# Kernel tuning notes

Hardware: AMD Instinct MI355X
Metric: run time of the kernel (lower is better)

The kernel has to match this reference:

```python
import jax, jax.numpy as jnp
import numpy as np

DIM = 1024
HEADS = 16
DIM_HEAD = 64
INNER = HEADS * DIM_HEAD  # 1024
RANK = 16
ALPHA = 8.0
LORA_SCALE = ALPHA / RANK  # 0.5
NUM_PATCHES = 256
NUM_FRAMES = 8
T = NUM_PATCHES * NUM_FRAMES  # 2048
B = 2
MEM = 16
EPS = 1e-5


def _block_causal_mask(num_patches, num_frames):
    # generate_mask_matrix: causal across frames, full within a frame
    tril = np.tril(np.ones((num_frames, num_frames), dtype=np.int32))
    m = np.kron(tril, np.ones((num_patches, num_patches), dtype=np.int32))
    return jnp.asarray(m[None, None])  # [1,1,T,T]


def setup_inputs() -> dict:
    key = jax.random.key(0)
    ks = jax.random.split(key, 16)
    s_in = 1.0 / np.sqrt(DIM)
    s_r = 1.0 / np.sqrt(RANK)
    return {
        "x": jax.random.normal(ks[0], (B, T, DIM), jnp.float32),
        "memory_tokens": jax.random.normal(ks[1], (B, MEM, DIM), jnp.float32),
        "ln_g": jnp.ones((DIM,), jnp.float32),
        "ln_b": jnp.zeros((DIM,), jnp.float32),
        "w_qkv": jax.random.normal(ks[2], (DIM, 3 * INNER), jnp.float32) * s_in,
        "qA": jax.random.normal(ks[3], (DIM, RANK), jnp.float32) * s_in,
        "qB": jax.random.normal(ks[4], (RANK, INNER), jnp.float32) * s_r * 0.02,
        "kA": jax.random.normal(ks[5], (DIM, RANK), jnp.float32) * s_in,
        "kB": jax.random.normal(ks[6], (RANK, INNER), jnp.float32) * s_r * 0.02,
        "vA": jax.random.normal(ks[7], (DIM, RANK), jnp.float32) * s_in,
        "vB": jax.random.normal(ks[8], (RANK, INNER), jnp.float32) * s_r * 0.02,
        "w_out": jax.random.normal(ks[9], (INNER, DIM), jnp.float32) / np.sqrt(INNER),
        "b_out": jnp.zeros((DIM,), jnp.float32),
        "outA": jax.random.normal(ks[10], (INNER, RANK), jnp.float32) / np.sqrt(INNER),
        "outB": jax.random.normal(ks[11], (RANK, DIM), jnp.float32) * s_r * 0.02,
        "bias_mask": _block_causal_mask(NUM_PATCHES, NUM_FRAMES),
    }


def _lora(x, A, Bm):
    return LORA_SCALE * ((x @ A) @ Bm)


def reference(x, memory_tokens, ln_g, ln_b, w_qkv, qA, qB, kA, kB, vA, vB,
              w_out, b_out, outA, outB, bias_mask):
    # LayerNorm
    mu = jnp.mean(x, axis=-1, keepdims=True)
    var = jnp.var(x, axis=-1, keepdims=True)
    xn = (x - mu) * jax.lax.rsqrt(var + EPS) * ln_g + ln_b

    qkv = xn @ w_qkv  # [B,T,3*INNER]
    q, k, v = jnp.split(qkv, 3, axis=-1)
    # LoRA deltas (memory_tokens enables the LoRA path)
    q = q + _lora(xn, qA, qB)
    k = k + _lora(xn, kA, kB)
    v = v + _lora(xn, vA, vB)

    def to_heads(t):
        b, n, _ = t.shape
        return t.reshape(b, n, HEADS, DIM_HEAD).transpose(0, 2, 1, 3)  # b h n d

    q, k, v = to_heads(q), to_heads(k), to_heads(v)
    scale = DIM_HEAD ** -0.5
    dots = jnp.einsum('bhid,bhjd->bhij', q, k) * scale  # [B,H,T,T]
    dots = jnp.where(bias_mask[:, :, :q.shape[2], :q.shape[2]] == 0, -jnp.inf, dots)
    attn = jax.nn.softmax(dots, axis=-1)  # dropout p=0.0
    out = jnp.einsum('bhij,bhjd->bhid', attn, v)
    out = out.transpose(0, 2, 1, 3).reshape(x.shape[0], x.shape[1], INNER)
    out = out @ w_out + b_out
    out = out + _lora(out, outA, outB)  # lora_on_out
    return out
```

## Files before the change

### kernel.cpp

```cpp
#include <hip/hip_runtime.h>


#define DIMSZ 1024
#define TSEQ  2048
#define MTOK  4096

typedef __attribute__((ext_vector_type(8))) short bf16x8;
typedef __attribute__((ext_vector_type(4))) short bf16x4;
typedef __attribute__((ext_vector_type(4))) float f32x4;

__device__ __forceinline__ unsigned short f2bf(float f) {
  unsigned int u = __float_as_uint(f);
  u += 0x7fffu + ((u >> 16) & 1u);
  return (unsigned short)(u >> 16);
}
__device__ __forceinline__ float bf2f(unsigned short s) {
  return __uint_as_float(((unsigned int)s) << 16);
}
__device__ __forceinline__ unsigned int cvtpk_bf16(float a, float b) {
  unsigned int d;
  asm("v_cvt_pk_bf16_f32 %0, %1, %2" : "=v"(d) : "v"(a), "v"(b));
  return d;
}
__device__ __forceinline__ void gload16(const void* g, void* l) {
  __builtin_amdgcn_global_load_lds((const __attribute__((address_space(1))) void*)g,
                                   (__attribute__((address_space(3))) void*)l, 16, 0, 0);
}

__global__ __launch_bounds__(256) void ln_kernel(const float* __restrict__ x,
    const float* __restrict__ g, const float* __restrict__ b,
    unsigned short* __restrict__ xn) {
  int row = blockIdx.x;
  int tid = threadIdx.x;
  const float4* xr = (const float4*)(x + (size_t)row * DIMSZ);
  float4 v = xr[tid];
  float s  = v.x + v.y + v.z + v.w;
  float s2 = v.x*v.x + v.y*v.y + v.z*v.z + v.w*v.w;
  #pragma unroll
  for (int off = 32; off > 0; off >>= 1) {
    s  += __shfl_xor(s, off, 64);
    s2 += __shfl_xor(s2, off, 64);
  }
  __shared__ float red[8];
  int wid = tid >> 6, lane = tid & 63;
  if (lane == 0) { red[wid] = s; red[wid + 4] = s2; }
  __syncthreads();
  s  = red[0] + red[1] + red[2] + red[3];
  s2 = red[4] + red[5] + red[6] + red[7];
  float mu  = s * (1.0f / DIMSZ);
  float var = s2 * (1.0f / DIMSZ) - mu * mu;
  float rstd = rsqrtf(var + 1e-5f);
  float4 gg = ((const float4*)g)[tid];
  float4 bb = ((const float4*)b)[tid];
  ushort4 o;
  o.x = f2bf((v.x - mu) * rstd * gg.x + bb.x);
  o.y = f2bf((v.y - mu) * rstd * gg.y + bb.y);
  o.z = f2bf((v.z - mu) * rstd * gg.z + bb.z);
  o.w = f2bf((v.w - mu) * rstd * gg.w + bb.w);
  ((ushort4*)(xn + (size_t)row * DIMSZ))[tid] = o;
}

__global__ __launch_bounds__(64) void woutA_kernel(const float* __restrict__ w_out,
    const float* __restrict__ outA, float* __restrict__ WA) {
  int k = blockIdx.x;
  int l = threadIdx.x;
  float a[16];
  #pragma unroll
  for (int r = 0; r < 16; ++r) a[r] = 0.f;
  for (int c = l; c < DIMSZ; c += 64) {
    float w = w_out[(size_t)k * DIMSZ + c];
    const float* ap = outA + (size_t)c * 16;
    #pragma unroll
    for (int r = 0; r < 16; ++r) a[r] += w * ap[r];
  }
  #pragma unroll
  for (int r = 0; r < 16; ++r) {
    #pragma unroll
    for (int off = 32; off > 0; off >>= 1) a[r] += __shfl_xor(a[r], off, 64);
  }
  if (l < 16) WA[k * 16 + l] = a[l];
}

__global__ __launch_bounds__(256) void beff_kernel(const float* __restrict__ b_out,
    const float* __restrict__ outA, const float* __restrict__ outB,
    float* __restrict__ beff) {
  int tid = threadIdx.x, wid = tid >> 6, lane = tid & 63;
  float a[16];
  #pragma unroll
  for (int r = 0; r < 16; ++r) a[r] = 0.f;
  for (int c = tid; c < DIMSZ; c += 256) {
    float bo = b_out[c];
    const float* ap = outA + (size_t)c * 16;
    #pragma unroll
    for (int r = 0; r < 16; ++r) a[r] += bo * ap[r];
  }
  #pragma unroll
  for (int r = 0; r < 16; ++r) {
    #pragma unroll
    for (int off = 32; off > 0; off >>= 1) a[r] += __shfl_xor(a[r], off, 64);
  }
  __shared__ float sh[4][16];
  if (lane == 0) {
    #pragma unroll
    for (int r = 0; r < 16; ++r) sh[wid][r] = a[r];
  }
  __syncthreads();
  __shared__ float tt[16];
  if (tid < 16) tt[tid] = sh[0][tid] + sh[1][tid] + sh[2][tid] + sh[3][tid];
  __syncthreads();
  for (int n = tid; n < DIMSZ; n += 256) {
    float l = 0.f;
    #pragma unroll
    for (int r = 0; r < 16; ++r) l += tt[r] * outB[(size_t)r * DIMSZ + n];
    beff[n] = b_out[n] + 0.5f * l;
  }
}

__global__ __launch_bounds__(256) void foldT4_kernel(
    const float* __restrict__ w_qkv, const float* __restrict__ w_out,
    const float* __restrict__ qA, const float* __restrict__ qB,
    const float* __restrict__ kA, const float* __restrict__ kB,
    const float* __restrict__ vA, const float* __restrict__ vB,
    const float* __restrict__ WA, const float* __restrict__ outB,
    unsigned short* __restrict__ WqkvT, unsigned short* __restrict__ WoutT) {
  __shared__ float Bs[16][64];
  __shared__ unsigned short Ts[64][72];
  int z = blockIdx.z;
  const float *W, *A, *Bf;
  unsigned short* Wt;
  int ldw, col_off;
  if (z == 0)      { W = w_qkv; ldw = 3072; col_off = 0;    A = qA; Bf = qB;   Wt = WqkvT; }
  else if (z == 1) { W = w_qkv; ldw = 3072; col_off = 1024; A = kA; Bf = kB;   Wt = WqkvT + 1048576; }
  else if (z == 2) { W = w_qkv; ldw = 3072; col_off = 2048; A = vA; Bf = vB;   Wt = WqkvT + 2097152; }
  else             { W = w_out; ldw = 1024; col_off = 0;    A = WA; Bf = outB; Wt = WoutT; }
  int n0 = blockIdx.x * 64, k0 = blockIdx.y * 64;
  int tx = threadIdx.x, ty = threadIdx.y;
  for (int r = ty; r < 16; r += 4) Bs[r][tx] = Bf[(size_t)r * DIMSZ + n0 + tx];
  __syncthreads();
  for (int k = ty; k < 64; k += 4) {
    int kk = k0 + k;
    float w = W[(size_t)kk * ldw + col_off + n0 + tx];
    const float* Ar = A + (size_t)kk * 16;
    float lora = 0.f;
    #pragma unroll
    for (int r = 0; r < 16; ++r) lora += Ar[r] * Bs[r][tx];
    Ts[tx][k] = f2bf(w + 0.5f * lora);
  }
  __syncthreads();
  for (int n = ty; n < 64; n += 4)
    Wt[(size_t)(n0 + n) * DIMSZ + k0 + tx] = Ts[n][tx];
}

template<int MODE>
__global__ __launch_bounds__(256) void gemm_kernel(
    const unsigned short* __restrict__ Abf, const unsigned short* __restrict__ Bt,
    int K,
    unsigned short* __restrict__ Qo, unsigned short* __restrict__ Ko,
    unsigned short* __restrict__ Vto,
    const float* __restrict__ bias, float* __restrict__ Cout) {
  __shared__ __align__(16) char As[128 * 64 * 2];
  __shared__ __align__(16) char Bs[128 * 64 * 2];
  int n0 = blockIdx.x * 128;
  int m0 = blockIdx.y * 128;
  int tid = threadIdx.x;
  int wid = tid >> 6, lane = tid & 63;
  int wr = wid >> 1, wc = wid & 1;
  int hi = lane >> 4;
  f32x4 acc[4][4];
  #pragma unroll
  for (int i = 0; i < 4; ++i)
    #pragma unroll
    for (int j = 0; j < 4; ++j) acc[i][j] = (f32x4){0.f, 0.f, 0.f, 0.f};

  const char* gA = (const char*)Abf;
  const char* gB = (const char*)Bt;
  int Kb2 = K * 2;
  int nkt = K >> 6;
  for (int kt = 0; kt < nkt; ++kt) {
    #pragma unroll
    for (int j = 0; j < 4; ++j) {
      int it = wid * 4 + j;
      int p = it * 1024 + lane * 16;
      int row = p >> 7, colb = p & 127;
      int L = colb ^ ((row & 7) << 4);
      gload16(gA + (size_t)(m0 + row) * Kb2 + kt * 128 + L, As + it * 1024);
      gload16(gB + (size_t)(n0 + row) * Kb2 + kt * 128 + L, Bs + it * 1024);
    }
    __syncthreads();
    #pragma unroll
    for (int ks = 0; ks < 2; ++ks) {
      int kb = ks * 64 + hi * 16;
      bf16x8 af[4], bfr[4];
      #pragma unroll
      for (int m = 0; m < 4; ++m) {
        int row = wr * 64 + m * 16 + (lane & 15);
        af[m] = *(const bf16x8*)(As + row * 128 + (kb ^ ((row & 7) << 4)));
      }
      #pragma unroll
      for (int n = 0; n < 4; ++n) {
        int row = wc * 64 + n * 16 + (lane & 15);
        bfr[n] = *(const bf16x8*)(Bs + row * 128 + (kb ^ ((row & 7) << 4)));
      }
      __builtin_amdgcn_s_setprio(1);
      #pragma unroll
      for (int n = 0; n < 4; ++n)
        #pragma unroll
        for (int m = 0; m < 4; ++m)
          acc[n][m] = __builtin_amdgcn_mfma_f32_16x16x32_bf16(bfr[n], af[m], acc[n][m], 0, 0, 0);
      __builtin_amdgcn_s_setprio(0);
    }
    __syncthreads();
  }

  if (MODE == 0) {
    int sec  = n0 >> 10;
    int nloc = (n0 & 1023) + wc * 64;
    int h = nloc >> 6;
    int mbase = m0 + wr * 64;
    #pragma unroll
    for (int m = 0; m < 4; ++m) {
      int gm = mbase + m * 16 + (lane & 15);
      int bb = gm >> 11, t = gm & 2047;
      #pragma unroll
      for (int n = 0; n < 4; ++n) {
        int dloc = n * 16 + hi * 4;
        if (sec == 2) {
          #pragma unroll
          for (int r = 0; r < 4; ++r)
            Vto[((size_t)((bb * 16 + h) * 64 + dloc + r)) * TSEQ + t] = f2bf(acc[n][m][r]);
        } else {
          bf16x4 o;
          #pragma unroll
          for (int r = 0; r < 4; ++r) o[r] = (short)f2bf(acc[n][m][r]);
          size_t idx = ((size_t)(bb * 16 + h) * TSEQ + t) * 64 + dloc;
          *(bf16x4*)((sec == 0 ? Qo : Ko) + idx) = o;
        }
      }
    }
  } else {
    int mbase = m0 + wr * 64;
    int nbase = n0 + wc * 64;
    #pragma unroll
    for (int m = 0; m < 4; ++m) {
      int t = mbase + m * 16 + (lane & 15);
      #pragma unroll
      for (int n = 0; n < 4; ++n) {
        int c = nbase + n * 16 + hi * 4;
        float4 bs = *(const float4*)(bias + c);
        float4 o;
        o.x = acc[n][m][0] + bs.x;
        o.y = acc[n][m][1] + bs.y;
        o.z = acc[n][m][2] + bs.z;
        o.w = acc[n][m][3] + bs.w;
        *(float4*)(Cout + (size_t)t * DIMSZ + c) = o;
      }
    }
  }
}

__global__ __launch_bounds__(256, 4) void attn_kernel(
    const unsigned short* __restrict__ Qg, const unsigned short* __restrict__ Kg,
    const unsigned short* __restrict__ Vt, unsigned short* __restrict__ Orow) {
  __shared__ __align__(16) char KsB[2][64 * 128];
  __shared__ __align__(16) char VsB[2][64 * 128];
  __shared__ __align__(16) char Ps[4][16 * 128];
  int bh = blockIdx.x;
  int y  = blockIdx.y;
  int qt = (y < 16) ? (31 - y) : (y - 16);
  int b = bh >> 4, h = bh & 15;
  int tid = threadIdx.x, wid = tid >> 6, lane = tid & 63;
  int hi = lane >> 4, lo = lane & 15;
  const char* Qb = (const char*)(Qg + (size_t)bh * TSEQ * 64);
  const char* Kb = (const char*)(Kg + (size_t)bh * TSEQ * 64);
  const char* Vb = (const char*)(Vt + (size_t)bh * 64 * TSEQ);
  int q0 = qt * 64;

  int srow = tid >> 3;
  int scol = ((tid & 7) << 4) ^ ((srow & 7) << 4);

  const float qscale = 0.18033688f;
  bf16x8 qf[2];
  {
    int row = q0 + wid * 16 + lo;
    #pragma unroll
    for (int ks = 0; ks < 2; ++ks) {
      bf16x8 raw = *(const bf16x8*)(Qb + (size_t)row * 128 + ks * 64 + hi * 16);
      bf16x8 sc;
      #pragma unroll
      for (int i = 0; i < 8; ++i)
        sc[i] = (short)f2bf(bf2f((unsigned short)raw[i]) * qscale);
      qf[ks] = sc;
    }
  }

  f32x4 Oacc[4];
  #pragma unroll
  for (int df = 0; df < 4; ++df) Oacc[df] = (f32x4){0.f, 0.f, 0.f, 0.f};
  float mrun = -INFINITY, lrun = 0.f;

  char* Pw = Ps[wid];
  char* pbase = Pw + lo * 128;
  int pswz = (lo & 7) << 4;

  int nkt = ((qt >> 2) + 1) << 2;

  {
    const char* ksrc = Kb + (size_t)srow * 128 + scol;
    gload16(ksrc,               KsB[0] + tid * 16);
    gload16(ksrc + 32 * 128,    KsB[0] + tid * 16 + 4096);
    const char* vsrc = Vb + (size_t)srow * (TSEQ * 2) + scol;
    gload16(vsrc,               VsB[0] + tid * 16);
    gload16(vsrc + 32 * (TSEQ * 2), VsB[0] + tid * 16 + 4096);
  }

  for (int kt = 0; kt < nkt; ++kt) {
    __syncthreads();
    if (kt + 1 < nkt) {
      int k0n = (kt + 1) << 6;
      char* kd = KsB[(kt + 1) & 1];
      const char* ksrc = Kb + (size_t)(k0n + srow) * 128 + scol;
      gload16(ksrc,            kd + tid * 16);
      gload16(ksrc + 32 * 128, kd + tid * 16 + 4096);
    }
    if (kt) {
      char* vd = VsB[kt & 1];
      const char* vsrc = Vb + (size_t)srow * (TSEQ * 2) + (kt << 7) + scol;
      gload16(vsrc,                   vd + tid * 16);
      gload16(vsrc + 32 * (TSEQ * 2), vd + tid * 16 + 4096);
    }
    const char* Kbuf = KsB[kt & 1];

    f32x4 s[4];
    #pragma unroll
    for (int nf = 0; nf < 4; ++nf) s[nf] = (f32x4){0.f, 0.f, 0.f, 0.f};
    #pragma unroll
    for (int ks = 0; ks < 2; ++ks) {
      int kb = ks * 64 + hi * 16;
      bf16x8 kf[4];
      #pragma unroll
      for (int nf = 0; nf < 4; ++nf) {
        int row = nf * 16 + lo;
        kf[nf] = *(const bf16x8*)(Kbuf + row * 128 + (kb ^ ((row & 7) << 4)));
      }
      __builtin_amdgcn_s_setprio(1);
      #pragma unroll
      for (int nf = 0; nf < 4; ++nf)
        s[nf] = __builtin_amdgcn_mfma_f32_16x16x32_bf16(kf[nf], qf[ks], s[nf], 0, 0, 0);
      __builtin_amdgcn_s_setprio(0);
    }

    if (kt) {
      const char* Vbuf = VsB[(kt - 1) & 1];
      #pragma unroll
      for (int ks2 = 0; ks2 < 2; ++ks2) {
        int kb = ks2 * 64 + hi * 16;
        bf16x8 pf = *(const bf16x8*)(Pw + lo * 128 + (kb ^ pswz));
        bf16x8 vf[4];
        #pragma unroll
        for (int df = 0; df < 4; ++df) {
          int row = df * 16 + lo;
          vf[df] = *(const bf16x8*)(Vbuf + row * 128 + (kb ^ ((row & 7) << 4)));
        }
        __builtin_amdgcn_s_setprio(1);
        #pragma unroll
        for (int df = 0; df < 4; ++df)
          Oacc[df] = __builtin_amdgcn_mfma_f32_16x16x32_bf16(vf[df], pf, Oacc[df], 0, 0, 0);
        __builtin_amdgcn_s_setprio(0);
      }
    }

    float a0 = fmaxf(fmaxf(s[0][0], s[0][1]), fmaxf(s[0][2], s[0][3]));
    float a1 = fmaxf(fmaxf(s[1][0], s[1][1]), fmaxf(s[1][2], s[1][3]));
    float a2 = fmaxf(fmaxf(s[2][0], s[2][1]), fmaxf(s[2][2], s[2][3]));
    float a3 = fmaxf(fmaxf(s[3][0], s[3][1]), fmaxf(s[3][2], s[3][3]));
    float mx = fmaxf(fmaxf(a0, a1), fmaxf(a2, a3));
    mx = fmaxf(mx, __shfl_xor(mx, 16, 64));
    mx = fmaxf(mx, __shfl_xor(mx, 32, 64));

    if (!__all(mx <= mrun + 8.0f)) {
      float mn = fmaxf(mrun, mx);
      float al = exp2f(mrun - mn);
      mrun = mn;
      lrun *= al;
      #pragma unroll
      for (int df = 0; df < 4; ++df)
        #pragma unroll
        for (int r = 0; r < 4; ++r) Oacc[df][r] *= al;
    }

    float rs0 = 0.f, rs1 = 0.f, rs2 = 0.f, rs3 = 0.f;
    #pragma unroll
    for (int nf = 0; nf < 4; ++nf) {
      float p0 = exp2f(s[nf][0] - mrun);
      float p1 = exp2f(s[nf][1] - mrun);
      float p2 = exp2f(s[nf][2] - mrun);
      float p3 = exp2f(s[nf][3] - mrun);
      s[nf][0] = p0; s[nf][1] = p1; s[nf][2] = p2; s[nf][3] = p3;
      rs0 += p0; rs1 += p1; rs2 += p2; rs3 += p3;
    }
    lrun += (rs0 + rs1) + (rs2 + rs3);

    #pragma unroll
    for (int nf = 0; nf < 4; ++nf) {
      unsigned int w0 = cvtpk_bf16(s[nf][0], s[nf][1]);
      unsigned int w1 = cvtpk_bf16(s[nf][2], s[nf][3]);
      uint2 pr; pr.x = w0; pr.y = w1;
      *(uint2*)(pbase + ((nf * 32 + hi * 8) ^ pswz)) = pr;
    }
  }

  __syncthreads();
  {
    const char* Vbuf = VsB[(nkt - 1) & 1];
    #pragma unroll
    for (int ks2 = 0; ks2 < 2; ++ks2) {
      int kb = ks2 * 64 + hi * 16;
      bf16x8 pf = *(const bf16x8*)(Pw + lo * 128 + (kb ^ pswz));
      bf16x8 vf[4];
      #pragma unroll
      for (int df = 0; df < 4; ++df) {
        int row = df * 16 + lo;
        vf[df] = *(const bf16x8*)(Vbuf + row * 128 + (kb ^ ((row & 7) << 4)));
      }
      __builtin_amdgcn_s_setprio(1);
      #pragma unroll
      for (int df = 0; df < 4; ++df)
        Oacc[df] = __builtin_amdgcn_mfma_f32_16x16x32_bf16(vf[df], pf, Oacc[df], 0, 0, 0);
      __builtin_amdgcn_s_setprio(0);
    }
  }

  lrun += __shfl_xor(lrun, 16, 64);
  lrun += __shfl_xor(lrun, 32, 64);
  float inv = 1.0f / lrun;
  int t = q0 + wid * 16 + lo;
  size_t rowbase = ((size_t)(b * TSEQ + t)) * DIMSZ + h * 64;
  #pragma unroll
  for (int df = 0; df < 4; ++df) {
    bf16x4 o;
    #pragma unroll
    for (int r = 0; r < 4; ++r) o[r] = (short)f2bf(Oacc[df][r] * inv);
    *(bf16x4*)(Orow + rowbase + df * 16 + hi * 4) = o;
  }
}

extern "C" void kernel_launch(void* const* d_in, const int* in_sizes, int n_in,
                              void* d_out, int out_size, void* d_ws, size_t ws_size,
                              hipStream_t stream) {
  (void)in_sizes; (void)n_in; (void)out_size; (void)ws_size;
  const float* x     = (const float*)d_in[0];
  const float* ln_g  = (const float*)d_in[2];
  const float* ln_b  = (const float*)d_in[3];
  const float* w_qkv = (const float*)d_in[4];
  const float* qA    = (const float*)d_in[5];
  const float* qB    = (const float*)d_in[6];
  const float* kA    = (const float*)d_in[7];
  const float* kB    = (const float*)d_in[8];
  const float* vA    = (const float*)d_in[9];
  const float* vB    = (const float*)d_in[10];
  const float* w_out = (const float*)d_in[11];
  const float* b_out = (const float*)d_in[12];
  const float* outA  = (const float*)d_in[13];
  const float* outB  = (const float*)d_in[14];

  char* ws = (char*)d_ws;
  unsigned short* xn    = (unsigned short*)(ws);
  unsigned short* WqkvT = (unsigned short*)(ws + 8388608);
  unsigned short* WoutT = (unsigned short*)(ws + 14680064);
  float*          WA    = (float*)(ws + 16777216);
  float*          beff  = (float*)(ws + 16842752);
  unsigned short* Qb    = (unsigned short*)(ws + 16846848);
  unsigned short* Kb    = (unsigned short*)(ws + 25235456);
  unsigned short* Vtb   = (unsigned short*)(ws + 33624064);
  unsigned short* Orow  = xn;
  float* outp = (float*)d_out;

  ln_kernel<<<MTOK, 256, 0, stream>>>(x, ln_g, ln_b, xn);
  woutA_kernel<<<DIMSZ, 64, 0, stream>>>(w_out, outA, WA);
  beff_kernel<<<1, 256, 0, stream>>>(b_out, outA, outB, beff);
  dim3 fb(64, 4);
  foldT4_kernel<<<dim3(16, 16, 4), fb, 0, stream>>>(w_qkv, w_out, qA, qB, kA, kB,
                                                    vA, vB, WA, outB, WqkvT, WoutT);

  gemm_kernel<0><<<dim3(24, 32), 256, 0, stream>>>(xn, WqkvT, DIMSZ, Qb, Kb, Vtb, nullptr, nullptr);
  attn_kernel<<<dim3(32, 32), 256, 0, stream>>>(Qb, Kb, Vtb, Orow);
  gemm_kernel<1><<<dim3(8, 32), 256, 0, stream>>>(Orow, WoutT, DIMSZ, nullptr, nullptr, nullptr, beff, outp);
}
```

Measured before the change: 142.9 us.

## Use 32x32 MFMA in attention with two waves per block, fuse prep kernels

The attention kernel is restructured so each of two waves handles 32 query rows using 32x32x16 bf16 MFMAs instead of four waves using 16x16x32. This cuts the number of MFMA issues and cross-lane reductions, but raises per-wave register pressure and halves threads per block, which changes occupancy. Separately, the LayerNorm, W_out·outA and effective-bias kernels are merged into one launch to save launch overhead.

```diff
diff --git a/kernel.cpp b/kernel.cpp
--- a/kernel.cpp
+++ b/kernel.cpp
@@ -8,6 +8,7 @@
 typedef __attribute__((ext_vector_type(8))) short bf16x8;
 typedef __attribute__((ext_vector_type(4))) short bf16x4;
 typedef __attribute__((ext_vector_type(4))) float f32x4;
+typedef __attribute__((ext_vector_type(16))) float f32x16;
 
 __device__ __forceinline__ unsigned short f2bf(float f) {
   unsigned int u = __float_as_uint(f);
@@ -27,92 +28,88 @@
                                    (__attribute__((address_space(3))) void*)l, 16, 0, 0);
 }
 
-__global__ __launch_bounds__(256) void ln_kernel(const float* __restrict__ x,
-    const float* __restrict__ g, const float* __restrict__ b,
-    unsigned short* __restrict__ xn) {
-  int row = blockIdx.x;
-  int tid = threadIdx.x;
-  const float4* xr = (const float4*)(x + (size_t)row * DIMSZ);
-  float4 v = xr[tid];
-  float s  = v.x + v.y + v.z + v.w;
-  float s2 = v.x*v.x + v.y*v.y + v.z*v.z + v.w*v.w;
-  #pragma unroll
-  for (int off = 32; off > 0; off >>= 1) {
-    s  += __shfl_xor(s, off, 64);
-    s2 += __shfl_xor(s2, off, 64);
-  }
+__global__ __launch_bounds__(256) void prep_kernel(const float* __restrict__ x,
+    const float* __restrict__ g, const float* __restrict__ bln,
+    const float* __restrict__ w_out, const float* __restrict__ outA,
+    const float* __restrict__ b_out, const float* __restrict__ outB,
+    unsigned short* __restrict__ xn, float* __restrict__ WA,
+    float* __restrict__ beff) {
   __shared__ float red[8];
-  int wid = tid >> 6, lane = tid & 63;
-  if (lane == 0) { red[wid] = s; red[wid + 4] = s2; }
-  __syncthreads();
-  s  = red[0] + red[1] + red[2] + red[3];
-  s2 = red[4] + red[5] + red[6] + red[7];
-  float mu  = s * (1.0f / DIMSZ);
-  float var = s2 * (1.0f / DIMSZ) - mu * mu;
-  float rstd = rsqrtf(var + 1e-5f);
-  float4 gg = ((const float4*)g)[tid];
-  float4 bb = ((const float4*)b)[tid];
-  ushort4 o;
-  o.x = f2bf((v.x - mu) * rstd * gg.x + bb.x);
-  o.y = f2bf((v.y - mu) * rstd * gg.y + bb.y);
-  o.z = f2bf((v.z - mu) * rstd * gg.z + bb.z);
-  o.w = f2bf((v.w - mu) * rstd * gg.w + bb.w);
-  ((ushort4*)(xn + (size_t)row * DIMSZ))[tid] = o;
-}
-
-__global__ __launch_bounds__(64) void woutA_kernel(const float* __restrict__ w_out,
-    const float* __restrict__ outA, float* __restrict__ WA) {
-  int k = blockIdx.x;
-  int l = threadIdx.x;
-  float a[16];
-  #pragma unroll
-  for (int r = 0; r < 16; ++r) a[r] = 0.f;
-  for (int c = l; c < DIMSZ; c += 64) {
-    float w = w_out[(size_t)k * DIMSZ + c];
-    const float* ap = outA + (size_t)c * 16;
-    #pragma unroll
-    for (int r = 0; r < 16; ++r) a[r] += w * ap[r];
-  }
-  #pragma unroll
-  for (int r = 0; r < 16; ++r) {
-    #pragma unroll
-    for (int off = 32; off > 0; off >>= 1) a[r] += __shfl_xor(a[r], off, 64);
-  }
-  if (l < 16) WA[k * 16 + l] = a[l];
-}
-
-__global__ __launch_bounds__(256) void beff_kernel(const float* __restrict__ b_out,
-    const float* __restrict__ outA, const float* __restrict__ outB,
-    float* __restrict__ beff) {
+  __shared__ float sh[4][16];
+  __shared__ float tt[16];
+  int bid = blockIdx.x;
   int tid = threadIdx.x, wid = tid >> 6, lane = tid & 63;
-  float a[16];
-  #pragma unroll
-  for (int r = 0; r < 16; ++r) a[r] = 0.f;
-  for (int c = tid; c < DIMSZ; c += 256) {
-    float bo = b_out[c];
-    const float* ap = outA + (size_t)c * 16;
-    #pragma unroll
-    for (int r = 0; r < 16; ++r) a[r] += bo * ap[r];
-  }
-  #pragma unroll
-  for (int r = 0; r < 16; ++r) {
-    #pragma unroll
-    for (int off = 32; off > 0; off >>= 1) a[r] += __shfl_xor(a[r], off, 64);
-  }
-  __shared__ float sh[4][16];
-  if (lane == 0) {
-    #pragma unroll
-    for (int r = 0; r < 16; ++r) sh[wid][r] = a[r];
-  }
-  __syncthreads();
-  __shared__ float tt[16];
-  if (tid < 16) tt[tid] = sh[0][tid] + sh[1][tid] + sh[2][tid] + sh[3][tid];
-  __syncthreads();
-  for (int n = tid; n < DIMSZ; n += 256) {
-    float l = 0.f;
-    #pragma unroll
-    for (int r = 0; r < 16; ++r) l += tt[r] * outB[(size_t)r * DIMSZ + n];
-    beff[n] = b_out[n] + 0.5f * l;
+  if (bid < MTOK) {
+    int row = bid;
+    const float4* xr = (const float4*)(x + (size_t)row * DIMSZ);
+    float4 v = xr[tid];
+    float s  = v.x + v.y + v.z + v.w;
+    float s2 = v.x*v.x + v.y*v.y + v.z*v.z + v.w*v.w;
+    #pragma unroll
+    for (int off = 32; off > 0; off >>= 1) {
+      s  += __shfl_xor(s, off, 64);
+      s2 += __shfl_xor(s2, off, 64);
+    }
+    if (lane == 0) { red[wid] = s; red[wid + 4] = s2; }
+    __syncthreads();
+    s  = red[0] + red[1] + red[2] + red[3];
+    s2 = red[4] + red[5] + red[6] + red[7];
+    float mu  = s * (1.0f / DIMSZ);
+    float var = s2 * (1.0f / DIMSZ) - mu * mu;
+    float rstd = rsqrtf(var + 1e-5f);
+    float4 gg = ((const float4*)g)[tid];
+    float4 bb = ((const float4*)bln)[tid];
+    ushort4 o;
+    o.x = f2bf((v.x - mu) * rstd * gg.x + bb.x);
+    o.y = f2bf((v.y - mu) * rstd * gg.y + bb.y);
+    o.z = f2bf((v.z - mu) * rstd * gg.z + bb.z);
+    o.w = f2bf((v.w - mu) * rstd * gg.w + bb.w);
+    ((ushort4*)(xn + (size_t)row * DIMSZ))[tid] = o;
+  } else if (bid < MTOK + 256) {
+    int k = (bid - MTOK) * 4 + wid;
+    float a[16];
+    #pragma unroll
+    for (int r = 0; r < 16; ++r) a[r] = 0.f;
+    for (int c = lane; c < DIMSZ; c += 64) {
+      float w = w_out[(size_t)k * DIMSZ + c];
+      const float* ap = outA + (size_t)c * 16;
+      #pragma unroll
+      for (int r = 0; r < 16; ++r) a[r] += w * ap[r];
+    }
+    #pragma unroll
+    for (int r = 0; r < 16; ++r) {
+      #pragma unroll
+      for (int off = 32; off > 0; off >>= 1) a[r] += __shfl_xor(a[r], off, 64);
+    }
+    if (lane < 16) WA[k * 16 + lane] = a[lane];
+  } else {
+    float a[16];
+    #pragma unroll
+    for (int r = 0; r < 16; ++r) a[r] = 0.f;
+    for (int c = tid; c < DIMSZ; c += 256) {
+      float bo = b_out[c];
+      const float* ap = outA + (size_t)c * 16;
+      #pragma unroll
+      for (int r = 0; r < 16; ++r) a[r] += bo * ap[r];
+    }
+    #pragma unroll
+    for (int r = 0; r < 16; ++r) {
+      #pragma unroll
+      for (int off = 32; off > 0; off >>= 1) a[r] += __shfl_xor(a[r], off, 64);
+    }
+    if (lane == 0) {
+      #pragma unroll
+      for (int r = 0; r < 16; ++r) sh[wid][r] = a[r];
+    }
+    __syncthreads();
+    if (tid < 16) tt[tid] = sh[0][tid] + sh[1][tid] + sh[2][tid] + sh[3][tid];
+    __syncthreads();
+    for (int n = tid; n < DIMSZ; n += 256) {
+      float l = 0.f;
+      #pragma unroll
+      for (int r = 0; r < 16; ++r) l += tt[r] * outB[(size_t)r * DIMSZ + n];
+      beff[n] = b_out[n] + 0.5f * l;
+    }
   }
 }
 
@@ -258,123 +255,126 @@
   }
 }
 
-__global__ __launch_bounds__(256, 4) void attn_kernel(
+__global__ __launch_bounds__(128, 2) void attn_kernel(
     const unsigned short* __restrict__ Qg, const unsigned short* __restrict__ Kg,
     const unsigned short* __restrict__ Vt, unsigned short* __restrict__ Orow) {
   __shared__ __align__(16) char KsB[2][64 * 128];
   __shared__ __align__(16) char VsB[2][64 * 128];
-  __shared__ __align__(16) char Ps[4][16 * 128];
+  __shared__ __align__(16) char Pws[2][32 * 128];
   int bh = blockIdx.x;
   int y  = blockIdx.y;
   int qt = (y < 16) ? (31 - y) : (y - 16);
   int b = bh >> 4, h = bh & 15;
   int tid = threadIdx.x, wid = tid >> 6, lane = tid & 63;
-  int hi = lane >> 4, lo = lane & 15;
+  int l31 = lane & 31, hi1 = lane >> 5;
   const char* Qb = (const char*)(Qg + (size_t)bh * TSEQ * 64);
   const char* Kb = (const char*)(Kg + (size_t)bh * TSEQ * 64);
   const char* Vb = (const char*)(Vt + (size_t)bh * 64 * TSEQ);
   int q0 = qt * 64;
 
   int srow = tid >> 3;
-  int scol = ((tid & 7) << 4) ^ ((srow & 7) << 4);
+  int scs  = ((tid & 7) << 4) ^ ((srow & 7) << 4);
 
   const float qscale = 0.18033688f;
-  bf16x8 qf[2];
+  bf16x8 qf[4];
   {
-    int row = q0 + wid * 16 + lo;
-    #pragma unroll
-    for (int ks = 0; ks < 2; ++ks) {
-      bf16x8 raw = *(const bf16x8*)(Qb + (size_t)row * 128 + ks * 64 + hi * 16);
-      bf16x8 sc;
+    int qrow = q0 + wid * 32 + l31;
+    #pragma unroll
+    for (int kb = 0; kb < 4; ++kb) {
+      bf16x8 raw = *(const bf16x8*)(Qb + (size_t)qrow * 128 + kb * 32 + hi1 * 16);
+      bf16x8 scv;
       #pragma unroll
       for (int i = 0; i < 8; ++i)
-        sc[i] = (short)f2bf(bf2f((unsigned short)raw[i]) * qscale);
-      qf[ks] = sc;
-    }
-  }
-
-  f32x4 Oacc[4];
-  #pragma unroll
-  for (int df = 0; df < 4; ++df) Oacc[df] = (f32x4){0.f, 0.f, 0.f, 0.f};
+        scv[i] = (short)f2bf(bf2f((unsigned short)raw[i]) * qscale);
+      qf[kb] = scv;
+    }
+  }
+
+  f32x16 Oa[2];
+  Oa[0] = (f32x16)(0.f); Oa[1] = (f32x16)(0.f);
   float mrun = -INFINITY, lrun = 0.f;
 
-  char* Pw = Ps[wid];
-  char* pbase = Pw + lo * 128;
-  int pswz = (lo & 7) << 4;
+  char* Pw   = Pws[wid];
+  char* prow = Pw + l31 * 128;
+  int   pswz = (l31 & 7) << 4;
 
   int nkt = ((qt >> 2) + 1) << 2;
 
   {
-    const char* ksrc = Kb + (size_t)srow * 128 + scol;
-    gload16(ksrc,               KsB[0] + tid * 16);
-    gload16(ksrc + 32 * 128,    KsB[0] + tid * 16 + 4096);
-    const char* vsrc = Vb + (size_t)srow * (TSEQ * 2) + scol;
-    gload16(vsrc,               VsB[0] + tid * 16);
-    gload16(vsrc + 32 * (TSEQ * 2), VsB[0] + tid * 16 + 4096);
+    const char* ks = Kb + (size_t)srow * 128 + scs;
+    char* kd = KsB[0] + tid * 16;
+    gload16(ks, kd); gload16(ks + 2048, kd + 2048);
+    gload16(ks + 4096, kd + 4096); gload16(ks + 6144, kd + 6144);
+    const char* vs = Vb + (size_t)srow * (TSEQ * 2) + scs;
+    char* vd = VsB[0] + tid * 16;
+    gload16(vs, vd); gload16(vs + 16 * TSEQ * 2, vd + 2048);
+    gload16(vs + 32 * TSEQ * 2, vd + 4096); gload16(vs + 48 * TSEQ * 2, vd + 6144);
   }
 
   for (int kt = 0; kt < nkt; ++kt) {
     __syncthreads();
     if (kt + 1 < nkt) {
-      int k0n = (kt + 1) << 6;
-      char* kd = KsB[(kt + 1) & 1];
-      const char* ksrc = Kb + (size_t)(k0n + srow) * 128 + scol;
-      gload16(ksrc,            kd + tid * 16);
-      gload16(ksrc + 32 * 128, kd + tid * 16 + 4096);
+      char* kd = KsB[(kt + 1) & 1] + tid * 16;
+      const char* ks = Kb + (size_t)(((kt + 1) << 6) + srow) * 128 + scs;
+      gload16(ks, kd); gload16(ks + 2048, kd + 2048);
+      gload16(ks + 4096, kd + 4096); gload16(ks + 6144, kd + 6144);
     }
     if (kt) {
-      char* vd = VsB[kt & 1];
-      const char* vsrc = Vb + (size_t)srow * (TSEQ * 2) + (kt << 7) + scol;
-      gload16(vsrc,                   vd + tid * 16);
-      gload16(vsrc + 32 * (TSEQ * 2), vd + tid * 16 + 4096);
+      char* vd = VsB[kt & 1] + tid * 16;
+      const char* vs = Vb + (size_t)srow * (TSEQ * 2) + (kt << 7) + scs;
+      gload16(vs, vd); gload16(vs + 16 * TSEQ * 2, vd + 2048);
+      gload16(vs + 32 * TSEQ * 2, vd + 4096); gload16(vs + 48 * TSEQ * 2, vd + 6144);
     }
     const char* Kbuf = KsB[kt & 1];
-
-    f32x4 s[4];
-    #pragma unroll
-    for (int nf = 0; nf < 4; ++nf) s[nf] = (f32x4){0.f, 0.f, 0.f, 0.f};
-    #pragma unroll
-    for (int ks = 0; ks < 2; ++ks) {
-      int kb = ks * 64 + hi * 16;
+    int rswz = (l31 & 7) << 4;
+
+    f32x16 sg[2];
+    sg[0] = (f32x16)(0.f); sg[1] = (f32x16)(0.f);
+    #pragma unroll
+    for (int kg = 0; kg < 2; ++kg) {
+      const char* krow = Kbuf + (kg * 32 + l31) * 128;
       bf16x8 kf[4];
       #pragma unroll
-      for (int nf = 0; nf < 4; ++nf) {
-        int row = nf * 16 + lo;
-        kf[nf] = *(const bf16x8*)(Kbuf + row * 128 + (kb ^ ((row & 7) << 4)));
-      }
+      for (int kb = 0; kb < 4; ++kb)
+        kf[kb] = *(const bf16x8*)(krow + ((kb * 32 + hi1 * 16) ^ rswz));
       __builtin_amdgcn_s_setprio(1);
       #pragma unroll
-      for (int nf = 0; nf < 4; ++nf)
-        s[nf] = __builtin_amdgcn_mfma_f32_16x16x32_bf16(kf[nf], qf[ks], s[nf], 0, 0, 0);
+      for (int kb = 0; kb < 4; ++kb)
+        sg[kg] = __builtin_amdgcn_mfma_f32_32x32x16_bf16(kf[kb], qf[kb], sg[kg], 0, 0, 0);
       __builtin_amdgcn_s_setprio(0);
     }
 
     if (kt) {
       const char* Vbuf = VsB[(kt - 1) & 1];
-      #pragma unroll
-      for (int ks2 = 0; ks2 < 2; ++ks2) {
-        int kb = ks2 * 64 + hi * 16;
-        bf16x8 pf = *(const bf16x8*)(Pw + lo * 128 + (kb ^ pswz));
+      bf16x8 pfb[4];
+      #pragma unroll
+      for (int kb = 0; kb < 4; ++kb)
+        pfb[kb] = *(const bf16x8*)(prow + ((kb * 32 + hi1 * 16) ^ pswz));
+      #pragma unroll
+      for (int dg = 0; dg < 2; ++dg) {
+        const char* vrow = Vbuf + (dg * 32 + l31) * 128;
         bf16x8 vf[4];
         #pragma unroll
-        for (int df = 0; df < 4; ++df) {
-          int row = df * 16 + lo;
-          vf[df] = *(const bf16x8*)(Vbuf + row * 128 + (kb ^ ((row & 7) << 4)));
-        }
+        for (int kb = 0; kb < 4; ++kb)
+          vf[kb] = *(const bf16x8*)(vrow + ((kb * 32 + hi1 * 16) ^ rswz));
         __builtin_amdgcn_s_setprio(1);
         #pragma unroll
-        for (int df = 0; df < 4; ++df)
-          Oacc[df] = __builtin_amdgcn_mfma_f32_16x16x32_bf16(vf[df], pf, Oacc[df], 0, 0, 0);
+        for (int kb = 0; kb < 4; ++kb)
+          Oa[dg] = __builtin_amdgcn_mfma_f32_32x32x16_bf16(vf[kb], pfb[kb], Oa[dg], 0, 0, 0);
         __builtin_amdgcn_s_setprio(0);
       }
     }
 
-    float a0 = fmaxf(fmaxf(s[0][0], s[0][1]), fmaxf(s[0][2], s[0][3]));
-    float a1 = fmaxf(fmaxf(s[1][0], s[1][1]), fmaxf(s[1][2], s[1][3]));
-    float a2 = fmaxf(fmaxf(s[2][0], s[2][1]), fmaxf(s[2][2], s[2][3]));
-    float a3 = fmaxf(fmaxf(s[3][0], s[3][1]), fmaxf(s[3][2], s[3][3]));
-    float mx = fmaxf(fmaxf(a0, a1), fmaxf(a2, a3));
-    mx = fmaxf(mx, __shfl_xor(mx, 16, 64));
+    float m0a = fmaxf(fmaxf(sg[0][0], sg[0][1]), fmaxf(sg[0][2], sg[0][3]));
+    float m0b = fmaxf(fmaxf(sg[0][4], sg[0][5]), fmaxf(sg[0][6], sg[0][7]));
+    float m0c = fmaxf(fmaxf(sg[0][8], sg[0][9]), fmaxf(sg[0][10], sg[0][11]));
+    float m0d = fmaxf(fmaxf(sg[0][12], sg[0][13]), fmaxf(sg[0][14], sg[0][15]));
+    float m1a = fmaxf(fmaxf(sg[1][0], sg[1][1]), fmaxf(sg[1][2], sg[1][3]));
+    float m1b = fmaxf(fmaxf(sg[1][4], sg[1][5]), fmaxf(sg[1][6], sg[1][7]));
+    float m1c = fmaxf(fmaxf(sg[1][8], sg[1][9]), fmaxf(sg[1][10], sg[1][11]));
+    float m1d = fmaxf(fmaxf(sg[1][12], sg[1][13]), fmaxf(sg[1][14], sg[1][15]));
+    float mx = fmaxf(fmaxf(fmaxf(m0a, m0b), fmaxf(m0c, m0d)),
+                     fmaxf(fmaxf(m1a, m1b), fmaxf(m1c, m1d)));
     mx = fmaxf(mx, __shfl_xor(mx, 32, 64));
 
     if (!__all(mx <= mrun + 8.0f)) {
@@ -383,64 +383,78 @@
       mrun = mn;
       lrun *= al;
       #pragma unroll
-      for (int df = 0; df < 4; ++df)
+      for (int dg = 0; dg < 2; ++dg)
         #pragma unroll
-        for (int r = 0; r < 4; ++r) Oacc[df][r] *= al;
-    }
-
-    float rs0 = 0.f, rs1 = 0.f, rs2 = 0.f, rs3 = 0.f;
-    #pragma unroll
-    for (int nf = 0; nf < 4; ++nf) {
-      float p0 = exp2f(s[nf][0] - mrun);
-      float p1 = exp2f(s[nf][1] - mrun);
-      float p2 = exp2f(s[nf][2] - mrun);
-      float p3 = exp2f(s[nf][3] - mrun);
-      s[nf][0] = p0; s[nf][1] = p1; s[nf][2] = p2; s[nf][3] = p3;
-      rs0 += p0; rs1 += p1; rs2 += p2; rs3 += p3;
-    }
-    lrun += (rs0 + rs1) + (rs2 + rs3);
-
-    #pragma unroll
-    for (int nf = 0; nf < 4; ++nf) {
-      unsigned int w0 = cvtpk_bf16(s[nf][0], s[nf][1]);
-      unsigned int w1 = cvtpk_bf16(s[nf][2], s[nf][3]);
-      uint2 pr; pr.x = w0; pr.y = w1;
-      *(uint2*)(pbase + ((nf * 32 + hi * 8) ^ pswz)) = pr;
+        for (int r = 0; r < 16; ++r) Oa[dg][r] *= al;
+    }
+
+    #pragma unroll
+    for (int kg = 0; kg < 2; ++kg) {
+      float rs0 = 0.f, rs1 = 0.f, rs2 = 0.f, rs3 = 0.f;
+      #pragma unroll
+      for (int r = 0; r < 4; ++r) {
+        float p0 = exp2f(sg[kg][4 * r + 0] - mrun);
+        float p1 = exp2f(sg[kg][4 * r + 1] - mrun);
+        float p2 = exp2f(sg[kg][4 * r + 2] - mrun);
+        float p3 = exp2f(sg[kg][4 * r + 3] - mrun);
+        sg[kg][4 * r + 0] = p0; sg[kg][4 * r + 1] = p1;
+        sg[kg][4 * r + 2] = p2; sg[kg][4 * r + 3] = p3;
+        rs0 += p0; rs1 += p1; rs2 += p2; rs3 += p3;
+      }
+      lrun += (rs0 + rs1) + (rs2 + rs3);
+      int base = kg * 64 + 8 * hi1;
+      uint2 w;
+      w.x = cvtpk_bf16(sg[kg][0], sg[kg][1]);
+      w.y = cvtpk_bf16(sg[kg][2], sg[kg][3]);
+      *(uint2*)(prow + ((base +  0) ^ pswz)) = w;
+      w.x = cvtpk_bf16(sg[kg][4], sg[kg][5]);
+      w.y = cvtpk_bf16(sg[kg][6], sg[kg][7]);
+      *(uint2*)(prow + ((base + 16) ^ pswz)) = w;
+      w.x = cvtpk_bf16(sg[kg][8], sg[kg][9]);
+      w.y = cvtpk_bf16(sg[kg][10], sg[kg][11]);
+      *(uint2*)(prow + ((base + 32) ^ pswz)) = w;
+      w.x = cvtpk_bf16(sg[kg][12], sg[kg][13]);
+      w.y = cvtpk_bf16(sg[kg][14], sg[kg][15]);
+      *(uint2*)(prow + ((base + 48) ^ pswz)) = w;
     }
   }
 
   __syncthreads();
   {
     const char* Vbuf = VsB[(nkt - 1) & 1];
-    #pragma unroll
-    for (int ks2 = 0; ks2 < 2; ++ks2) {
-      int kb = ks2 * 64 + hi * 16;
-      bf16x8 pf = *(const bf16x8*)(Pw + lo * 128 + (kb ^ pswz));
+    int rswz = (l31 & 7) << 4;
+    bf16x8 pfb[4];
+    #pragma unroll
+    for (int kb = 0; kb < 4; ++kb)
+      pfb[kb] = *(const bf16x8*)(prow + ((kb * 32 + hi1 * 16) ^ pswz));
+    #pragma unroll
+    for (int dg = 0; dg < 2; ++dg) {
+      const char* vrow = Vbuf + (dg * 32 + l31) * 128;
       bf16x8 vf[4];
       #pragma unroll
-      for (int df = 0; df < 4; ++df) {
-        int row = df * 16 + lo;
-        vf[df] = *(const bf16x8*)(Vbuf + row * 128 + (kb ^ ((row & 7) << 4)));
-      }
+      for (int kb = 0; kb < 4; ++kb)
+        vf[kb] = *(const bf16x8*)(vrow + ((kb * 32 + hi1 * 16) ^ rswz));
       __builtin_amdgcn_s_setprio(1);
       #pragma unroll
-      for (int df = 0; df < 4; ++df)
-        Oacc[df] = __builtin_amdgcn_mfma_f32_16x16x32_bf16(vf[df], pf, Oacc[df], 0, 0, 0);
+      for (int kb = 0; kb < 4; ++kb)
+        Oa[dg] = __builtin_amdgcn_mfma_f32_32x32x16_bf16(vf[kb], pfb[kb], Oa[dg], 0, 0, 0);
       __builtin_amdgcn_s_setprio(0);
     }
   }
 
-  lrun += __shfl_xor(lrun, 16, 64);
   lrun += __shfl_xor(lrun, 32, 64);
   float inv = 1.0f / lrun;
-  int t = q0 + wid * 16 + lo;
+  int t = q0 + wid * 32 + l31;
   size_t rowbase = ((size_t)(b * TSEQ + t)) * DIMSZ + h * 64;
   #pragma unroll
-  for (int df = 0; df < 4; ++df) {
-    bf16x4 o;
-    #pragma unroll
-    for (int r = 0; r < 4; ++r) o[r] = (short)f2bf(Oacc[df][r] * inv);
-    *(bf16x4*)(Orow + rowbase + df * 16 + hi * 4) = o;
+  for (int dg = 0; dg < 2; ++dg) {
+    #pragma unroll
+    for (int rr = 0; rr < 4; ++rr) {
+      uint2 w;
+      w.x = cvtpk_bf16(Oa[dg][4 * rr + 0] * inv, Oa[dg][4 * rr + 1] * inv);
+      w.y = cvtpk_bf16(Oa[dg][4 * rr + 2] * inv, Oa[dg][4 * rr + 3] * inv);
+      *(uint2*)(Orow + rowbase + dg * 32 + 8 * rr + 4 * hi1) = w;
+    }
   }
 }
 
@@ -475,14 +489,13 @@
   unsigned short* Orow  = xn;
   float* outp = (float*)d_out;
 
-  ln_kernel<<<MTOK, 256, 0, stream>>>(x, ln_g, ln_b, xn);
-  woutA_kernel<<<DIMSZ, 64, 0, stream>>>(w_out, outA, WA);
-  beff_kernel<<<1, 256, 0, stream>>>(b_out, outA, outB, beff);
+  prep_kernel<<<MTOK + 257, 256, 0, stream>>>(x, ln_g, ln_b, w_out, outA, b_out,
+                                              outB, xn, WA, beff);
   dim3 fb(64, 4);
   foldT4_kernel<<<dim3(16, 16, 4), fb, 0, stream>>>(w_qkv, w_out, qA, qB, kA, kB,
                                                     vA, vB, WA, outB, WqkvT, WoutT);
 
   gemm_kernel<0><<<dim3(24, 32), 256, 0, stream>>>(xn, WqkvT, DIMSZ, Qb, Kb, Vtb, nullptr, nullptr);
-  attn_kernel<<<dim3(32, 32), 256, 0, stream>>>(Qb, Kb, Vtb, Orow);
+  attn_kernel<<<dim3(32, 32), 128, 0, stream>>>(Qb, Kb, Vtb, Orow);
   gemm_kernel<1><<<dim3(8, 32), 256, 0, stream>>>(Orow, WoutT, DIMSZ, nullptr, nullptr, nullptr, beff, outp);
 }
```

Measured after the change: 151.6 us. +6.1%, slower.
